# Optimization experiments

Hardware: AMD Instinct MI355X
Metric: run time of the kernel (lower is better)

## Reference

```python
import jax, jax.numpy as jnp
import numpy as np

E, T, D, I, G, K = 8, 1024, 1024, 5632, 128, 2  # experts, tokens, hidden, intermediate, gptq group, topk
RENORMALIZE = True


def setup_inputs() -> dict:
    key = jax.random.key(0)
    ks = jax.random.split(key, 6)
    x = jax.random.normal(ks[0], (T, D), dtype=jnp.float32)
    gating_output = jax.random.normal(ks[1], (T, E), dtype=jnp.float32)
    # int4 GPTQ nibbles stored as int32 in [0, 16)
    w1_q = jax.random.randint(ks[2], (E, D, 2 * I), 0, 16, dtype=jnp.int32)
    w2_q = jax.random.randint(ks[3], (E, I, D), 0, 16, dtype=jnp.int32)
    # per-group scales (group size G along the input/contraction dim)
    w1_scale = jax.random.uniform(ks[4], (E, D // G, 2 * I), dtype=jnp.float32) * 0.02
    w2_scale = jax.random.uniform(ks[5], (E, I // G, D), dtype=jnp.float32) * 0.02
    return {"x": x, "gating_output": gating_output, "w1_q": w1_q, "w2_q": w2_q,
            "w1_scale": w1_scale, "w2_scale": w2_scale}


def _dequant(q, scale, group_size):
    # symmetric GPTQ int4: w = (q - 8) * scale, scale broadcast over its group
    s = jnp.repeat(scale, group_size, axis=1)  # [E, Kdim, N]
    return (q.astype(scale.dtype) - 8.0) * s


def reference(x, gating_output, w1_q, w2_q, w1_scale, w2_scale):
    w1 = _dequant(w1_q, w1_scale, G)  # [E, D, 2I]
    w2 = _dequant(w2_q, w2_scale, G)  # [E, I, D]

    # top-k softmax routing (use_grouped_topk=False path)
    probs = jax.nn.softmax(gating_output, axis=-1)        # [T, E]
    topk_w, topk_i = jax.lax.top_k(probs, K)              # [T, K]
    if RENORMALIZE:
        topk_w = topk_w / jnp.sum(topk_w, axis=-1, keepdims=True)
    # dense combine weights [T, E] (zero where expert not selected)
    cw = jnp.sum(jax.nn.one_hot(topk_i, E, dtype=x.dtype) * topk_w[..., None], axis=1)

    # expert MLPs: silu(x @ Wg) * (x @ Wu) @ Wd
    h = jnp.einsum('td,edn->etn', x, w1)                  # [E, T, 2I]
    gate, up = h[..., :I], h[..., I:]
    act = jax.nn.silu(gate) * up                          # [E, T, I]
    y = jnp.einsum('eti,eid->etd', act, w2)               # [E, T, D]

    out = jnp.einsum('te,etd->td', cw, y)                 # [T, D]
    return out
```

## Files before the change

kernel.cpp:

```cpp
#include <hip/hip_runtime.h>
#include <cstdint>
#include <cstddef>

#define E_ 8
#define T_ 1024
#define D_ 1024
#define I_ 5632
#define TWO_I_ 11264
#define NPAD_MAX 2176
#define NGRP_MAX 136

#define WS_ACTF_B 65536
#define WS_XGF_B  (65536 + 24510464)
#define WS_Y_B    WS_XGF_B
#define WS_CNT   0
#define WS_BASEP 8
#define WS_ESLOT 16
#define WS_TOKW  2064
#define WS_ETOK  4112

typedef __attribute__((ext_vector_type(8))) __bf16 bf16x8;
typedef __attribute__((ext_vector_type(4))) float  f32x4;

__device__ __forceinline__ unsigned f2bf(float f) {
    unsigned u = __float_as_uint(f);
    u += 0x7fffu + ((u >> 16) & 1u);
    return u >> 16;
}
__device__ __forceinline__ unsigned pack2bf(float f0, float f1) {
    unsigned a0 = __float_as_uint(f0); a0 += 0x7fffu + ((a0 >> 16) & 1u);
    unsigned a1 = __float_as_uint(f1); a1 += 0x7fffu + ((a1 >> 16) & 1u);
    return (a0 >> 16) | (a1 & 0xffff0000u);
}

__global__ void routing_kernel(const float* __restrict__ gate,
                               int* cnt, int* basep, int* eslot,
                               float* tokw, int* etok)
{
    int t = threadIdx.x;
    if (t < E_) cnt[t] = 0;
    __syncthreads();
    float g[E_];
#pragma unroll
    for (int e = 0; e < E_; ++e) g[e] = gate[t * E_ + e];
    int i0 = 0; float p0 = g[0];
#pragma unroll
    for (int e = 1; e < E_; ++e) if (g[e] > p0) { p0 = g[e]; i0 = e; }
    int i1 = -1; float p1 = -1e30f;
#pragma unroll
    for (int e = 0; e < E_; ++e) if (e != i0 && g[e] > p1) { p1 = g[e]; i1 = e; }
    float w0 = 1.0f / (1.0f + expf(p1 - p0));
    float w1 = 1.0f - w0;
    int s0 = atomicAdd(&cnt[i0], 1);
    int s1 = atomicAdd(&cnt[i1], 1);
    etok[i0 * T_ + s0] = t;
    etok[i1 * T_ + s1] = t;
    eslot[t * 2 + 0] = i0 * T_ + s0;  tokw[t * 2 + 0] = w0;
    eslot[t * 2 + 1] = i1 * T_ + s1;  tokw[t * 2 + 1] = w1;
    __syncthreads();
    if (t == 0) {
        int r = 0;
#pragma unroll
        for (int e = 0; e < E_; ++e) { basep[e] = r; r += (cnt[e] + 15) & ~15; }
    }
}

__global__ void gather_cast_kernel(const float* __restrict__ x,
                                   const int* __restrict__ cnt,
                                   const int* __restrict__ basep,
                                   const int* __restrict__ etok,
                                   unsigned short* __restrict__ xgf)
{
    int e = blockIdx.x >> 6, g = blockIdx.x & 63;
    int n = cnt[e];
    if (g * 16 >= n) return;
    int tid = threadIdx.x;
    int row = g * 16 + (tid & 15);
    row = min(row, n - 1);
    int tok = etok[e * T_ + row];
    const float* xr = x + (size_t)tok * D_;
    unsigned short* dst = xgf + ((size_t)(basep[e] >> 4) + g) * 16384;
#pragma unroll
    for (int it = 0; it < 8; ++it) {
        int c = it * 16 + (tid >> 4);
        float4 v0 = *(const float4*)(xr + c * 8);
        float4 v1 = *(const float4*)(xr + c * 8 + 4);
        uint4 h;
        h.x = pack2bf(v0.x, v0.y); h.y = pack2bf(v0.z, v0.w);
        h.z = pack2bf(v1.x, v1.y); h.w = pack2bf(v1.z, v1.w);
        *(uint4*)(dst + c * 128 + (tid & 15) * 8) = h;
    }
}

__global__ __launch_bounds__(512, 4) void gemm1_kernel(
    const unsigned short* __restrict__ xgf, const int* __restrict__ w1q,
    const float* __restrict__ w1s, const int* __restrict__ cnt,
    const int* __restrict__ basep, unsigned short* __restrict__ actf)
{
    __shared__ unsigned char blds[2][4096];
    int cg = blockIdx.x % 176, e = blockIdx.x / 176;
    int n = cnt[e];
    if (n <= 0) return;
    int npad = (n + 15) & ~15;
    int pb = basep[e];
    int tid = threadIdx.x, lane = tid & 63, w = tid >> 6;
    int l15 = lane & 15, lq = lane >> 4;
    int colg = w & 1, mh = w >> 1;
    int jcol = cg * 32 + colg * 16 + l15;

    int col64 = lane, kg = w;
    int jb = (col64 < 32) ? (cg * 32 + col64) : (I_ + cg * 32 + (col64 - 32));
    const int*   gq  = w1q + ((size_t)e * 1024 + kg * 4) * TWO_I_ + jb;
    const float* sqp = w1s + (size_t)e * 8 * TWO_I_ + jb;
    unsigned swr = (unsigned)(col64 >> 4) * 1024
                 + (unsigned)((kg >> 1) * 16 + (col64 & 15)) * 16
                 + (unsigned)(kg & 1) * 8;
    unsigned srd = (unsigned)colg * 1024 + (unsigned)lane * 16;

    int P0[4], P1[4], P2[4], P3[4];
    float S0, S1, S2, S3;

#define G1_ISSUE(S, P, SS)                                                  \
    { _Pragma("unroll")                                                     \
      for (int i_ = 0; i_ < 4; ++i_)                                        \
          P[i_] = gq[(size_t)((S) * 32 + i_) * TWO_I_];                     \
      SS = sqp[(size_t)((S) >> 2) * TWO_I_]; }

#define G1_DEQW(S, P, SS)                                                   \
    { float oc_ = -8.f * SS;                                                \
      uint2 fr_;                                                            \
      fr_.x = pack2bf((float)P[0]*SS + oc_, (float)P[1]*SS + oc_);          \
      fr_.y = pack2bf((float)P[2]*SS + oc_, (float)P[3]*SS + oc_);          \
      *(uint2*)(&blds[(S) & 1][swr]) = fr_; }

    for (int tb = 0; tb < npad; tb += 320) {
        int aoff[5];
#pragma unroll
        for (int mi = 0; mi < 5; ++mi) {
            int R = tb + mh * 80 + mi * 16;
            R = min(R, npad - 16);
            aoff[mi] = ((pb + R) >> 4) * 32768;
        }
        const char* abase = (const char*)xgf + lq * 256 + l15 * 16;

        f32x4 accg[5], accu[5];
#pragma unroll
        for (int mi = 0; mi < 5; ++mi) {
            accg[mi] = (f32x4){0.f, 0.f, 0.f, 0.f};
            accu[mi] = (f32x4){0.f, 0.f, 0.f, 0.f};
        }
        G1_ISSUE(0, P0, S0);
        G1_ISSUE(1, P1, S1);
        G1_ISSUE(2, P2, S2);
        G1_ISSUE(3, P3, S3);
        G1_DEQW(0, P0, S0);
        G1_ISSUE(4, P0, S0);
        asm volatile("s_waitcnt lgkmcnt(0)" ::: "memory");
        __builtin_amdgcn_s_barrier();
        asm volatile("" ::: "memory");

#pragma unroll 4
        for (int s = 0; s < 32; ++s) {
            const char* at = abase + (size_t)s * 1024;
            bf16x8 a[5];
#pragma unroll
            for (int mi = 0; mi < 5; ++mi)
                a[mi] = *(const bf16x8*)(at + aoff[mi]);
            if (s + 1 < 32) {
                const int sl = (s + 1) & 3;
                if (sl == 0)      { G1_DEQW(s+1, P0, S0); if (s+5 < 32) { G1_ISSUE(s+5, P0, S0); } }
                else if (sl == 1) { G1_DEQW(s+1, P1, S1); if (s+5 < 32) { G1_ISSUE(s+5, P1, S1); } }
                else if (sl == 2) { G1_DEQW(s+1, P2, S2); if (s+5 < 32) { G1_ISSUE(s+5, P2, S2); } }
                else              { G1_DEQW(s+1, P3, S3); if (s+5 < 32) { G1_ISSUE(s+5, P3, S3); } }
            }
            bf16x8 bg = *(const bf16x8*)(&blds[s & 1][srd]);
            bf16x8 bu = *(const bf16x8*)(&blds[s & 1][srd + 2048]);
#pragma unroll
            for (int mi = 0; mi < 5; ++mi) {
                accg[mi] = __builtin_amdgcn_mfma_f32_16x16x32_bf16(a[mi], bg, accg[mi], 0, 0, 0);
                accu[mi] = __builtin_amdgcn_mfma_f32_16x16x32_bf16(a[mi], bu, accu[mi], 0, 0, 0);
            }
            asm volatile("s_waitcnt lgkmcnt(0)" ::: "memory");
            __builtin_amdgcn_s_barrier();
            asm volatile("" ::: "memory");
        }
#pragma unroll
        for (int mi = 0; mi < 5; ++mi) {
#pragma unroll
            for (int r = 0; r < 4; ++r) {
                int ml = mh * 80 + mi * 16 + lq * 4 + r;
                int m = tb + ml;
                if (m < npad) {
                    float gv = accg[mi][r], uv = accu[mi][r];
                    float av = gv / (1.f + __expf(-gv)) * uv;
                    int prow = pb + m;
                    size_t o = (size_t)(prow >> 4) * 90112 + (jcol >> 3) * 128
                             + (prow & 15) * 8 + (jcol & 7);
                    actf[o] = (unsigned short)f2bf(av);
                }
            }
        }
    }
#undef G1_ISSUE
#undef G1_DEQW
}

__global__ __launch_bounds__(512, 4) void gemm2_kernel(
    const unsigned short* __restrict__ actf, const int* __restrict__ w2q,
    const float* __restrict__ w2s, const int* __restrict__ cnt,
    const int* __restrict__ basep, float* __restrict__ y)
{
    __shared__ unsigned char blds[2][4096];
    int bid = blockIdx.x;
    int seg = bid & 3, dt = (bid >> 2) & 15, e = bid >> 6;
    int n = cnt[e];
    if (n <= 0) return;
    int npad = (n + 15) & ~15;
    int pb = basep[e];
    int tid = threadIdx.x, lane = tid & 63, w = tid >> 6;
    int l15 = lane & 15, lq = lane >> 4;
    int colg = w & 1, mh = w >> 1;
    int dcol = dt * 64 + colg * 32 + l15;

    int col64 = lane, kg = w;
    int colb = dt * 64 + col64;
    const int*   gq  = w2q + ((size_t)e * 5632 + seg * 1408 + kg * 4) * 1024 + colb;
    const float* sqp = w2s + ((size_t)e * 44 + seg * 11) * 1024 + colb;
    unsigned swr = (unsigned)(col64 >> 4) * 1024
                 + (unsigned)((kg >> 1) * 16 + (col64 & 15)) * 16
                 + (unsigned)(kg & 1) * 8;
    unsigned srd = (unsigned)colg * 2048 + (unsigned)lane * 16;

    int P0[4], P1[4], P2[4], P3[4];
    float S0, S1, S2, S3;

#define G2_ISSUE(S, P, SS)                                                  \
    { _Pragma("unroll")                                                     \
      for (int i_ = 0; i_ < 4; ++i_)                                        \
          P[i_] = gq[(size_t)((S) * 32 + i_) * 1024];                       \
      SS = sqp[(size_t)((S) >> 2) * 1024]; }

#define G2_DEQW(S, P, SS)                                                   \
    { float oc_ = -8.f * SS;                                                \
      uint2 fr_;                                                            \
      fr_.x = pack2bf((float)P[0]*SS + oc_, (float)P[1]*SS + oc_);          \
      fr_.y = pack2bf((float)P[2]*SS + oc_, (float)P[3]*SS + oc_);          \
      *(uint2*)(&blds[(S) & 1][swr]) = fr_; }

    for (int tb = 0; tb < npad; tb += 320) {
        int aoff[5];
#pragma unroll
        for (int mi = 0; mi < 5; ++mi) {
            int R = tb + mh * 80 + mi * 16;
            R = min(R, npad - 16);
            aoff[mi] = ((pb + R) >> 4) * 180224;
        }
        const char* abase = (const char*)actf + seg * 45056 + lq * 256 + l15 * 16;

        f32x4 acc0[5], acc1[5];
#pragma unroll
        for (int mi = 0; mi < 5; ++mi) {
            acc0[mi] = (f32x4){0.f, 0.f, 0.f, 0.f};
            acc1[mi] = (f32x4){0.f, 0.f, 0.f, 0.f};
        }
        G2_ISSUE(0, P0, S0);
        G2_ISSUE(1, P1, S1);
        G2_ISSUE(2, P2, S2);
        G2_ISSUE(3, P3, S3);
        G2_DEQW(0, P0, S0);
        G2_ISSUE(4, P0, S0);
        asm volatile("s_waitcnt lgkmcnt(0)" ::: "memory");
        __builtin_amdgcn_s_barrier();
        asm volatile("" ::: "memory");

#pragma unroll 4
        for (int s = 0; s < 44; ++s) {
            const char* at = abase + (size_t)s * 1024;
            bf16x8 a[5];
#pragma unroll
            for (int mi = 0; mi < 5; ++mi)
                a[mi] = *(const bf16x8*)(at + aoff[mi]);
            if (s + 1 < 44) {
                const int sl = (s + 1) & 3;
                if (sl == 0)      { G2_DEQW(s+1, P0, S0); if (s+5 < 44) { G2_ISSUE(s+5, P0, S0); } }
                else if (sl == 1) { G2_DEQW(s+1, P1, S1); if (s+5 < 44) { G2_ISSUE(s+5, P1, S1); } }
                else if (sl == 2) { G2_DEQW(s+1, P2, S2); if (s+5 < 44) { G2_ISSUE(s+5, P2, S2); } }
                else              { G2_DEQW(s+1, P3, S3); if (s+5 < 44) { G2_ISSUE(s+5, P3, S3); } }
            }
            bf16x8 b0 = *(const bf16x8*)(&blds[s & 1][srd]);
            bf16x8 b1 = *(const bf16x8*)(&blds[s & 1][srd + 1024]);
#pragma unroll
            for (int mi = 0; mi < 5; ++mi) {
                acc0[mi] = __builtin_amdgcn_mfma_f32_16x16x32_bf16(a[mi], b0, acc0[mi], 0, 0, 0);
                acc1[mi] = __builtin_amdgcn_mfma_f32_16x16x32_bf16(a[mi], b1, acc1[mi], 0, 0, 0);
            }
            asm volatile("s_waitcnt lgkmcnt(0)" ::: "memory");
            __builtin_amdgcn_s_barrier();
            asm volatile("" ::: "memory");
        }
#pragma unroll
        for (int mi = 0; mi < 5; ++mi) {
#pragma unroll
            for (int r = 0; r < 4; ++r) {
                int m = tb + mh * 80 + mi * 16 + lq * 4 + r;
                if (m < n) {
                    float* yr = y + (size_t)seg * NPAD_MAX * 1024 + (size_t)(pb + m) * 1024;
                    yr[dcol]      = acc0[mi][r];
                    yr[dcol + 16] = acc1[mi][r];
                }
            }
        }
    }
#undef G2_ISSUE
#undef G2_DEQW
}

__global__ void combine_kernel(const float* __restrict__ y,
                               const int* __restrict__ eslot,
                               const float* __restrict__ tokw,
                               const int* __restrict__ basep,
                               float* __restrict__ out)
{
    int idx = blockIdx.x * blockDim.x + threadIdx.x;
    int t  = idx >> 8;
    int dc = idx & 255;
    int es0 = eslot[t * 2 + 0], es1 = eslot[t * 2 + 1];
    float w0 = tokw[t * 2 + 0], w1 = tokw[t * 2 + 1];
    int p0 = basep[es0 >> 10] + (es0 & 1023);
    int p1 = basep[es1 >> 10] + (es1 & 1023);
    const float4* y4 = (const float4*)y;
    float4 o = (float4){0.f, 0.f, 0.f, 0.f};
#pragma unroll
    for (int seg = 0; seg < 4; ++seg) {
        float4 a = y4[((size_t)seg * NPAD_MAX + p0) * 256 + dc];
        float4 b = y4[((size_t)seg * NPAD_MAX + p1) * 256 + dc];
        o.x += w0 * a.x + w1 * b.x;
        o.y += w0 * a.y + w1 * b.y;
        o.z += w0 * a.z + w1 * b.z;
        o.w += w0 * a.w + w1 * b.w;
    }
    ((float4*)out)[idx] = o;
}

extern "C" void kernel_launch(void* const* d_in, const int* in_sizes, int n_in,
                              void* d_out, int out_size, void* d_ws, size_t ws_size,
                              hipStream_t stream)
{
    const float* x    = (const float*)d_in[0];
    const float* gate = (const float*)d_in[1];
    const int*   w1q  = (const int*)d_in[2];
    const int*   w2q  = (const int*)d_in[3];
    const float* w1s  = (const float*)d_in[4];
    const float* w2s  = (const float*)d_in[5];
    float* out = (float*)d_out;
    int*   wsi = (int*)d_ws;
    float* wsf = (float*)d_ws;

    int*   cnt   = wsi + WS_CNT;
    int*   basep = wsi + WS_BASEP;
    int*   eslot = wsi + WS_ESLOT;
    float* tokw  = wsf + WS_TOKW;
    int*   etok  = wsi + WS_ETOK;
    unsigned short* actf = (unsigned short*)((char*)d_ws + WS_ACTF_B);
    unsigned short* xgf  = (unsigned short*)((char*)d_ws + WS_XGF_B);
    float*          y    = (float*)((char*)d_ws + WS_Y_B);

    routing_kernel<<<1, 1024, 0, stream>>>(gate, cnt, basep, eslot, tokw, etok);
    gather_cast_kernel<<<E_ * 64, 256, 0, stream>>>(x, cnt, basep, etok, xgf);
    gemm1_kernel<<<E_ * 176, 512, 0, stream>>>(xgf, w1q, w1s, cnt, basep, actf);
    gemm2_kernel<<<E_ * 16 * 4, 512, 0, stream>>>(actf, w2q, w2s, cnt, basep, y);
    combine_kernel<<<(T_ * D_ / 4) / 256, 256, 0, stream>>>(y, eslot, tokw, basep, out);
}
```

Measured before the change: 741.4 us.

## Widen GEMM tiles to 1024-thread blocks with vectorized weight loads and swizzled LDS

Both expert GEMMs move to 1024-thread blocks with wider column tiles (128+128 gate/up columns in gemm1, 256 output columns in gemm2). Each A fragment now feeds four MFMAs instead of two, raising reuse per activation load. Weight nibbles are fetched as int4 vectors with an XOR-swizzled LDS layout, and s_setprio is raised around the MFMA block. The prefetch depth is cut from four stages to two. gemm2 splits K into 8 segments instead of 4, so combine now reads 8 partial sums, which means more y traffic and fewer blocks for gemm1 (352).

Result: slower. 1.092 ms (+47.3%).

```diff
diff --git a/kernel.cpp b/kernel.cpp
--- a/kernel.cpp
+++ b/kernel.cpp
@@ -92,111 +92,129 @@
     }
 }
 
-__global__ __launch_bounds__(512, 4) void gemm1_kernel(
+__global__ __launch_bounds__(1024) void gemm1_kernel(
     const unsigned short* __restrict__ xgf, const int* __restrict__ w1q,
     const float* __restrict__ w1s, const int* __restrict__ cnt,
     const int* __restrict__ basep, unsigned short* __restrict__ actf)
 {
-    __shared__ unsigned char blds[2][4096];
-    int cg = blockIdx.x % 176, e = blockIdx.x / 176;
+    __shared__ unsigned char blds[2][16384];
+    int cg = blockIdx.x % 44, e = blockIdx.x / 44;
     int n = cnt[e];
     if (n <= 0) return;
     int npad = (n + 15) & ~15;
     int pb = basep[e];
     int tid = threadIdx.x, lane = tid & 63, w = tid >> 6;
     int l15 = lane & 15, lq = lane >> 4;
-    int colg = w & 1, mh = w >> 1;
-    int jcol = cg * 32 + colg * 16 + l15;
-
-    int col64 = lane, kg = w;
-    int jb = (col64 < 32) ? (cg * 32 + col64) : (I_ + cg * 32 + (col64 - 32));
-    const int*   gq  = w1q + ((size_t)e * 1024 + kg * 4) * TWO_I_ + jb;
+    int colg = w & 3, mh = w >> 2;
+
+    int colq = lane, kg = w;
+    int col0 = colq * 4;
+    int jb = (col0 < 128) ? (cg * 128 + col0) : (I_ + cg * 128 + (col0 - 128));
+    const int*   gq  = w1q + ((size_t)e * 1024 + kg) * TWO_I_ + jb;
     const float* sqp = w1s + (size_t)e * 8 * TWO_I_ + jb;
-    unsigned swr = (unsigned)(col64 >> 4) * 1024
-                 + (unsigned)((kg >> 1) * 16 + (col64 & 15)) * 16
-                 + (unsigned)(kg & 1) * 8;
-    unsigned srd = (unsigned)colg * 1024 + (unsigned)lane * 16;
-
-    int P0[4], P1[4], P2[4], P3[4];
-    float S0, S1, S2, S3;
-
-#define G1_ISSUE(S, P, SS)                                                  \
-    { _Pragma("unroll")                                                     \
-      for (int i_ = 0; i_ < 4; ++i_)                                        \
-          P[i_] = gq[(size_t)((S) * 32 + i_) * TWO_I_];                     \
-      SS = sqp[(size_t)((S) >> 2) * TWO_I_]; }
-
-#define G1_DEQW(S, P, SS)                                                   \
-    { float oc_ = -8.f * SS;                                                \
-      uint2 fr_;                                                            \
-      fr_.x = pack2bf((float)P[0]*SS + oc_, (float)P[1]*SS + oc_);          \
-      fr_.y = pack2bf((float)P[2]*SS + oc_, (float)P[3]*SS + oc_);          \
-      *(uint2*)(&blds[(S) & 1][swr]) = fr_; }
-
-    for (int tb = 0; tb < npad; tb += 320) {
-        int aoff[5];
-#pragma unroll
-        for (int mi = 0; mi < 5; ++mi) {
-            int R = tb + mh * 80 + mi * 16;
+    unsigned wb  = (unsigned)colq * 256 + (unsigned)(kg & 7) * 2;
+    unsigned ch0 = (unsigned)((((kg >> 3)    ) ^ (colq & 3)) << 4);
+    unsigned ch1 = (unsigned)((((kg >> 3) + 2) ^ (colq & 3)) << 4);
+    unsigned srdb = (unsigned)(colg * 16 + l15) * 64
+                  + (unsigned)(((lq ^ (l15 >> 2)) & 3) * 16);
+
+    int4  PA0, PA1, PB0, PB1;
+    float4 SA, SB;
+
+#define G1_ISSUE(S, P0, P1, SS)                                             \
+    { P0 = *(const int4*)(gq + (size_t)(S) * 32 * TWO_I_);                  \
+      P1 = *(const int4*)(gq + ((size_t)(S) * 32 + 16) * TWO_I_);           \
+      SS = *(const float4*)(sqp + (size_t)((S) >> 2) * TWO_I_); }
+
+#define G1_DEQW(S, P0, P1, SS)                                              \
+    { unsigned char* bp = &blds[(S) & 1][0];                                \
+      *(unsigned short*)(bp + wb +   0 + ch0) = (unsigned short)f2bf((float)P0.x * SS.x - 8.f * SS.x); \
+      *(unsigned short*)(bp + wb +  64 + ch0) = (unsigned short)f2bf((float)P0.y * SS.y - 8.f * SS.y); \
+      *(unsigned short*)(bp + wb + 128 + ch0) = (unsigned short)f2bf((float)P0.z * SS.z - 8.f * SS.z); \
+      *(unsigned short*)(bp + wb + 192 + ch0) = (unsigned short)f2bf((float)P0.w * SS.w - 8.f * SS.w); \
+      *(unsigned short*)(bp + wb +   0 + ch1) = (unsigned short)f2bf((float)P1.x * SS.x - 8.f * SS.x); \
+      *(unsigned short*)(bp + wb +  64 + ch1) = (unsigned short)f2bf((float)P1.y * SS.y - 8.f * SS.y); \
+      *(unsigned short*)(bp + wb + 128 + ch1) = (unsigned short)f2bf((float)P1.z * SS.z - 8.f * SS.z); \
+      *(unsigned short*)(bp + wb + 192 + ch1) = (unsigned short)f2bf((float)P1.w * SS.w - 8.f * SS.w); }
+
+    for (int tb = 0; tb < npad; tb += 256) {
+        int aoff[4];
+#pragma unroll
+        for (int mi = 0; mi < 4; ++mi) {
+            int R = tb + mh * 64 + mi * 16;
             R = min(R, npad - 16);
             aoff[mi] = ((pb + R) >> 4) * 32768;
         }
         const char* abase = (const char*)xgf + lq * 256 + l15 * 16;
 
-        f32x4 accg[5], accu[5];
-#pragma unroll
-        for (int mi = 0; mi < 5; ++mi) {
-            accg[mi] = (f32x4){0.f, 0.f, 0.f, 0.f};
-            accu[mi] = (f32x4){0.f, 0.f, 0.f, 0.f};
-        }
-        G1_ISSUE(0, P0, S0);
-        G1_ISSUE(1, P1, S1);
-        G1_ISSUE(2, P2, S2);
-        G1_ISSUE(3, P3, S3);
-        G1_DEQW(0, P0, S0);
-        G1_ISSUE(4, P0, S0);
+        f32x4 acc[4][4];
+#pragma unroll
+        for (int mi = 0; mi < 4; ++mi)
+#pragma unroll
+            for (int nf = 0; nf < 4; ++nf)
+                acc[mi][nf] = (f32x4){0.f, 0.f, 0.f, 0.f};
+
+        G1_ISSUE(0, PA0, PA1, SA);
+        G1_ISSUE(1, PB0, PB1, SB);
+        G1_DEQW(0, PA0, PA1, SA);
+        G1_ISSUE(2, PA0, PA1, SA);
         asm volatile("s_waitcnt lgkmcnt(0)" ::: "memory");
         __builtin_amdgcn_s_barrier();
         asm volatile("" ::: "memory");
 
-#pragma unroll 4
+#pragma unroll 2
         for (int s = 0; s < 32; ++s) {
             const char* at = abase + (size_t)s * 1024;
-            bf16x8 a[5];
-#pragma unroll
-            for (int mi = 0; mi < 5; ++mi)
+            bf16x8 a[4];
+#pragma unroll
+            for (int mi = 0; mi < 4; ++mi)
                 a[mi] = *(const bf16x8*)(at + aoff[mi]);
             if (s + 1 < 32) {
-                const int sl = (s + 1) & 3;
-                if (sl == 0)      { G1_DEQW(s+1, P0, S0); if (s+5 < 32) { G1_ISSUE(s+5, P0, S0); } }
-                else if (sl == 1) { G1_DEQW(s+1, P1, S1); if (s+5 < 32) { G1_ISSUE(s+5, P1, S1); } }
-                else if (sl == 2) { G1_DEQW(s+1, P2, S2); if (s+5 < 32) { G1_ISSUE(s+5, P2, S2); } }
-                else              { G1_DEQW(s+1, P3, S3); if (s+5 < 32) { G1_ISSUE(s+5, P3, S3); } }
-            }
-            bf16x8 bg = *(const bf16x8*)(&blds[s & 1][srd]);
-            bf16x8 bu = *(const bf16x8*)(&blds[s & 1][srd + 2048]);
-#pragma unroll
-            for (int mi = 0; mi < 5; ++mi) {
-                accg[mi] = __builtin_amdgcn_mfma_f32_16x16x32_bf16(a[mi], bg, accg[mi], 0, 0, 0);
-                accu[mi] = __builtin_amdgcn_mfma_f32_16x16x32_bf16(a[mi], bu, accu[mi], 0, 0, 0);
-            }
+                if ((s + 1) & 1) { G1_DEQW(s + 1, PB0, PB1, SB); }
+                else             { G1_DEQW(s + 1, PA0, PA1, SA); }
+            }
+            if (s + 3 < 32) {
+                if ((s + 3) & 1) { G1_ISSUE(s + 3, PB0, PB1, SB); }
+                else             { G1_ISSUE(s + 3, PA0, PA1, SA); }
+            }
+            const unsigned char* bp = &blds[s & 1][0];
+            bf16x8 b0 = *(const bf16x8*)(bp + srdb);
+            bf16x8 b1 = *(const bf16x8*)(bp + srdb + 4096);
+            bf16x8 b2 = *(const bf16x8*)(bp + srdb + 8192);
+            bf16x8 b3 = *(const bf16x8*)(bp + srdb + 12288);
+            __builtin_amdgcn_s_setprio(1);
+#pragma unroll
+            for (int mi = 0; mi < 4; ++mi) {
+                acc[mi][0] = __builtin_amdgcn_mfma_f32_16x16x32_bf16(a[mi], b0, acc[mi][0], 0, 0, 0);
+                acc[mi][1] = __builtin_amdgcn_mfma_f32_16x16x32_bf16(a[mi], b1, acc[mi][1], 0, 0, 0);
+                acc[mi][2] = __builtin_amdgcn_mfma_f32_16x16x32_bf16(a[mi], b2, acc[mi][2], 0, 0, 0);
+                acc[mi][3] = __builtin_amdgcn_mfma_f32_16x16x32_bf16(a[mi], b3, acc[mi][3], 0, 0, 0);
+            }
+            __builtin_amdgcn_s_setprio(0);
             asm volatile("s_waitcnt lgkmcnt(0)" ::: "memory");
             __builtin_amdgcn_s_barrier();
             asm volatile("" ::: "memory");
         }
 #pragma unroll
-        for (int mi = 0; mi < 5; ++mi) {
+        for (int mi = 0; mi < 4; ++mi) {
 #pragma unroll
             for (int r = 0; r < 4; ++r) {
-                int ml = mh * 80 + mi * 16 + lq * 4 + r;
-                int m = tb + ml;
+                int m = tb + mh * 64 + mi * 16 + lq * 4 + r;
                 if (m < npad) {
-                    float gv = accg[mi][r], uv = accu[mi][r];
-                    float av = gv / (1.f + __expf(-gv)) * uv;
                     int prow = pb + m;
-                    size_t o = (size_t)(prow >> 4) * 90112 + (jcol >> 3) * 128
-                             + (prow & 15) * 8 + (jcol & 7);
-                    actf[o] = (unsigned short)f2bf(av);
+                    size_t rg = (size_t)(prow >> 4) * 90112 + (prow & 15) * 8;
+                    {
+                        float gv = acc[mi][0][r], uv = acc[mi][2][r];
+                        float av = gv / (1.f + __expf(-gv)) * uv;
+                        int icol = cg * 128 + colg * 16 + l15;
+                        actf[rg + (icol >> 3) * 128 + (icol & 7)] = (unsigned short)f2bf(av);
+                    }
+                    {
+                        float gv = acc[mi][1][r], uv = acc[mi][3][r];
+                        float av = gv / (1.f + __expf(-gv)) * uv;
+                        int icol = cg * 128 + 64 + colg * 16 + l15;
+                        actf[rg + (icol >> 3) * 128 + (icol & 7)] = (unsigned short)f2bf(av);
+                    }
                 }
             }
         }
@@ -205,108 +223,121 @@
 #undef G1_DEQW
 }
 
-__global__ __launch_bounds__(512, 4) void gemm2_kernel(
+__global__ __launch_bounds__(1024) void gemm2_kernel(
     const unsigned short* __restrict__ actf, const int* __restrict__ w2q,
     const float* __restrict__ w2s, const int* __restrict__ cnt,
     const int* __restrict__ basep, float* __restrict__ y)
 {
-    __shared__ unsigned char blds[2][4096];
+    __shared__ unsigned char blds[2][16384];
     int bid = blockIdx.x;
-    int seg = bid & 3, dt = (bid >> 2) & 15, e = bid >> 6;
+    int seg = bid & 7, dt = (bid >> 3) & 3, e = bid >> 5;
     int n = cnt[e];
     if (n <= 0) return;
     int npad = (n + 15) & ~15;
     int pb = basep[e];
     int tid = threadIdx.x, lane = tid & 63, w = tid >> 6;
     int l15 = lane & 15, lq = lane >> 4;
-    int colg = w & 1, mh = w >> 1;
-    int dcol = dt * 64 + colg * 32 + l15;
-
-    int col64 = lane, kg = w;
-    int colb = dt * 64 + col64;
-    const int*   gq  = w2q + ((size_t)e * 5632 + seg * 1408 + kg * 4) * 1024 + colb;
-    const float* sqp = w2s + ((size_t)e * 44 + seg * 11) * 1024 + colb;
-    unsigned swr = (unsigned)(col64 >> 4) * 1024
-                 + (unsigned)((kg >> 1) * 16 + (col64 & 15)) * 16
-                 + (unsigned)(kg & 1) * 8;
-    unsigned srd = (unsigned)colg * 2048 + (unsigned)lane * 16;
-
-    int P0[4], P1[4], P2[4], P3[4];
-    float S0, S1, S2, S3;
-
-#define G2_ISSUE(S, P, SS)                                                  \
-    { _Pragma("unroll")                                                     \
-      for (int i_ = 0; i_ < 4; ++i_)                                        \
-          P[i_] = gq[(size_t)((S) * 32 + i_) * 1024];                       \
-      SS = sqp[(size_t)((S) >> 2) * 1024]; }
-
-#define G2_DEQW(S, P, SS)                                                   \
-    { float oc_ = -8.f * SS;                                                \
-      uint2 fr_;                                                            \
-      fr_.x = pack2bf((float)P[0]*SS + oc_, (float)P[1]*SS + oc_);          \
-      fr_.y = pack2bf((float)P[2]*SS + oc_, (float)P[3]*SS + oc_);          \
-      *(uint2*)(&blds[(S) & 1][swr]) = fr_; }
-
-    for (int tb = 0; tb < npad; tb += 320) {
-        int aoff[5];
-#pragma unroll
-        for (int mi = 0; mi < 5; ++mi) {
-            int R = tb + mh * 80 + mi * 16;
+    int colg = w & 3, mh = w >> 2;
+    int kbase = seg * 704;
+
+    int colq = lane, kg = w;
+    const int*   gq  = w2q + ((size_t)e * 5632 + kbase + kg) * 1024 + dt * 256 + colq * 4;
+    const float* sqp = w2s + (size_t)e * 44 * 1024 + dt * 256 + colq * 4;
+    unsigned wb  = (unsigned)colq * 256 + (unsigned)(kg & 7) * 2;
+    unsigned ch0 = (unsigned)((((kg >> 3)    ) ^ (colq & 3)) << 4);
+    unsigned ch1 = (unsigned)((((kg >> 3) + 2) ^ (colq & 3)) << 4);
+    unsigned srdb = (unsigned)(colg * 16 + l15) * 64
+                  + (unsigned)(((lq ^ (l15 >> 2)) & 3) * 16);
+
+    int4  PA0, PA1, PB0, PB1;
+    float4 SA, SB;
+
+#define G2_ISSUE(S, P0, P1, SS)                                             \
+    { P0 = *(const int4*)(gq + (size_t)(S) * 32 * 1024);                    \
+      P1 = *(const int4*)(gq + ((size_t)(S) * 32 + 16) * 1024);             \
+      SS = *(const float4*)(sqp + (size_t)((kbase + (S) * 32) >> 7) * 1024); }
+
+#define G2_DEQW(S, P0, P1, SS)                                              \
+    { unsigned char* bp = &blds[(S) & 1][0];                                \
+      *(unsigned short*)(bp + wb +   0 + ch0) = (unsigned short)f2bf((float)P0.x * SS.x - 8.f * SS.x); \
+      *(unsigned short*)(bp + wb +  64 + ch0) = (unsigned short)f2bf((float)P0.y * SS.y - 8.f * SS.y); \
+      *(unsigned short*)(bp + wb + 128 + ch0) = (unsigned short)f2bf((float)P0.z * SS.z - 8.f * SS.z); \
+      *(unsigned short*)(bp + wb + 192 + ch0) = (unsigned short)f2bf((float)P0.w * SS.w - 8.f * SS.w); \
+      *(unsigned short*)(bp + wb +   0 + ch1) = (unsigned short)f2bf((float)P1.x * SS.x - 8.f * SS.x); \
+      *(unsigned short*)(bp + wb +  64 + ch1) = (unsigned short)f2bf((float)P1.y * SS.y - 8.f * SS.y); \
+      *(unsigned short*)(bp + wb + 128 + ch1) = (unsigned short)f2bf((float)P1.z * SS.z - 8.f * SS.z); \
+      *(unsigned short*)(bp + wb + 192 + ch1) = (unsigned short)f2bf((float)P1.w * SS.w - 8.f * SS.w); }
+
+    for (int tb = 0; tb < npad; tb += 256) {
+        int aoff[4];
+#pragma unroll
+        for (int mi = 0; mi < 4; ++mi) {
+            int R = tb + mh * 64 + mi * 16;
             R = min(R, npad - 16);
             aoff[mi] = ((pb + R) >> 4) * 180224;
         }
-        const char* abase = (const char*)actf + seg * 45056 + lq * 256 + l15 * 16;
-
-        f32x4 acc0[5], acc1[5];
-#pragma unroll
-        for (int mi = 0; mi < 5; ++mi) {
-            acc0[mi] = (f32x4){0.f, 0.f, 0.f, 0.f};
-            acc1[mi] = (f32x4){0.f, 0.f, 0.f, 0.f};
-        }
-        G2_ISSUE(0, P0, S0);
-        G2_ISSUE(1, P1, S1);
-        G2_ISSUE(2, P2, S2);
-        G2_ISSUE(3, P3, S3);
-        G2_DEQW(0, P0, S0);
-        G2_ISSUE(4, P0, S0);
+        const char* abase = (const char*)actf + seg * 22528 + lq * 256 + l15 * 16;
+
+        f32x4 acc[4][4];
+#pragma unroll
+        for (int mi = 0; mi < 4; ++mi)
+#pragma unroll
+            for (int nf = 0; nf < 4; ++nf)
+                acc[mi][nf] = (f32x4){0.f, 0.f, 0.f, 0.f};
+
+        G2_ISSUE(0, PA0, PA1, SA);
+        G2_ISSUE(1, PB0, PB1, SB);
+        G2_DEQW(0, PA0, PA1, SA);
+        G2_ISSUE(2, PA0, PA1, SA);
         asm volatile("s_waitcnt lgkmcnt(0)" ::: "memory");
         __builtin_amdgcn_s_barrier();
         asm volatile("" ::: "memory");
 
-#pragma unroll 4
-        for (int s = 0; s < 44; ++s) {
+#pragma unroll 2
+        for (int s = 0; s < 22; ++s) {
             const char* at = abase + (size_t)s * 1024;
-            bf16x8 a[5];
-#pragma unroll
-            for (int mi = 0; mi < 5; ++mi)
+            bf16x8 a[4];
+#pragma unroll
+            for (int mi = 0; mi < 4; ++mi)
                 a[mi] = *(const bf16x8*)(at + aoff[mi]);
-            if (s + 1 < 44) {
-                const int sl = (s + 1) & 3;
-                if (sl == 0)      { G2_DEQW(s+1, P0, S0); if (s+5 < 44) { G2_ISSUE(s+5, P0, S0); } }
-                else if (sl == 1) { G2_DEQW(s+1, P1, S1); if (s+5 < 44) { G2_ISSUE(s+5, P1, S1); } }
-                else if (sl == 2) { G2_DEQW(s+1, P2, S2); if (s+5 < 44) { G2_ISSUE(s+5, P2, S2); } }
-                else              { G2_DEQW(s+1, P3, S3); if (s+5 < 44) { G2_ISSUE(s+5, P3, S3); } }
-            }
-            bf16x8 b0 = *(const bf16x8*)(&blds[s & 1][srd]);
-            bf16x8 b1 = *(const bf16x8*)(&blds[s & 1][srd + 1024]);
-#pragma unroll
-            for (int mi = 0; mi < 5; ++mi) {
-                acc0[mi] = __builtin_amdgcn_mfma_f32_16x16x32_bf16(a[mi], b0, acc0[mi], 0, 0, 0);
-                acc1[mi] = __builtin_amdgcn_mfma_f32_16x16x32_bf16(a[mi], b1, acc1[mi], 0, 0, 0);
-            }
+            if (s + 1 < 22) {
+                if ((s + 1) & 1) { G2_DEQW(s + 1, PB0, PB1, SB); }
+                else             { G2_DEQW(s + 1, PA0, PA1, SA); }
+            }
+            if (s + 3 < 22) {
+                if ((s + 3) & 1) { G2_ISSUE(s + 3, PB0, PB1, SB); }
+                else             { G2_ISSUE(s + 3, PA0, PA1, SA); }
+            }
+            const unsigned char* bp = &blds[s & 1][0];
+            bf16x8 b0 = *(const bf16x8*)(bp + srdb);
+            bf16x8 b1 = *(const bf16x8*)(bp + srdb + 4096);
+            bf16x8 b2 = *(const bf16x8*)(bp + srdb + 8192);
+            bf16x8 b3 = *(const bf16x8*)(bp + srdb + 12288);
+            __builtin_amdgcn_s_setprio(1);
+#pragma unroll
+            for (int mi = 0; mi < 4; ++mi) {
+                acc[mi][0] = __builtin_amdgcn_mfma_f32_16x16x32_bf16(a[mi], b0, acc[mi][0], 0, 0, 0);
+                acc[mi][1] = __builtin_amdgcn_mfma_f32_16x16x32_bf16(a[mi], b1, acc[mi][1], 0, 0, 0);
+                acc[mi][2] = __builtin_amdgcn_mfma_f32_16x16x32_bf16(a[mi], b2, acc[mi][2], 0, 0, 0);
+                acc[mi][3] = __builtin_amdgcn_mfma_f32_16x16x32_bf16(a[mi], b3, acc[mi][3], 0, 0, 0);
+            }
+            __builtin_amdgcn_s_setprio(0);
             asm volatile("s_waitcnt lgkmcnt(0)" ::: "memory");
             __builtin_amdgcn_s_barrier();
             asm volatile("" ::: "memory");
         }
 #pragma unroll
-        for (int mi = 0; mi < 5; ++mi) {
+        for (int mi = 0; mi < 4; ++mi) {
 #pragma unroll
             for (int r = 0; r < 4; ++r) {
-                int m = tb + mh * 80 + mi * 16 + lq * 4 + r;
+                int m = tb + mh * 64 + mi * 16 + lq * 4 + r;
                 if (m < n) {
-                    float* yr = y + (size_t)seg * NPAD_MAX * 1024 + (size_t)(pb + m) * 1024;
-                    yr[dcol]      = acc0[mi][r];
-                    yr[dcol + 16] = acc1[mi][r];
+                    float* yr = y + ((size_t)seg * NPAD_MAX + pb + m) * 1024;
+                    int dc = dt * 256 + colg * 16 + l15;
+                    yr[dc]       = acc[mi][0][r];
+                    yr[dc + 64]  = acc[mi][1][r];
+                    yr[dc + 128] = acc[mi][2][r];
+                    yr[dc + 192] = acc[mi][3][r];
                 }
             }
         }
@@ -331,7 +362,7 @@
     const float4* y4 = (const float4*)y;
     float4 o = (float4){0.f, 0.f, 0.f, 0.f};
 #pragma unroll
-    for (int seg = 0; seg < 4; ++seg) {
+    for (int seg = 0; seg < 8; ++seg) {
         float4 a = y4[((size_t)seg * NPAD_MAX + p0) * 256 + dc];
         float4 b = y4[((size_t)seg * NPAD_MAX + p1) * 256 + dc];
         o.x += w0 * a.x + w1 * b.x;
@@ -367,7 +398,7 @@
 
     routing_kernel<<<1, 1024, 0, stream>>>(gate, cnt, basep, eslot, tokw, etok);
     gather_cast_kernel<<<E_ * 64, 256, 0, stream>>>(x, cnt, basep, etok, xgf);
-    gemm1_kernel<<<E_ * 176, 512, 0, stream>>>(xgf, w1q, w1s, cnt, basep, actf);
-    gemm2_kernel<<<E_ * 16 * 4, 512, 0, stream>>>(actf, w2q, w2s, cnt, basep, y);
+    gemm1_kernel<<<E_ * 44, 1024, 0, stream>>>(xgf, w1q, w1s, cnt, basep, actf);
+    gemm2_kernel<<<E_ * 4 * 8, 1024, 0, stream>>>(actf, w2q, w2s, cnt, basep, y);
     combine_kernel<<<(T_ * D_ / 4) / 256, 256, 0, stream>>>(y, eslot, tokw, basep, out);
 }
```
